# Optimization experiments

Measured on AMD Instinct MI355X. Metric: run time of the kernel, lower is better.

## Reference

```python
import jax, jax.numpy as jnp
import numpy as np

EMBED_DIM = 1024
NUM_HEADS = 16
SEQ = 2048
BATCH = 2


def setup_inputs() -> dict:
    key = jax.random.key(0)
    ks = jax.random.split(key, 9)
    E = EMBED_DIM
    gain = 1.0 / np.sqrt(2.0)  # xavier_uniform with gain 1/sqrt(2) (qkv_same_dim)
    limit = gain * np.sqrt(6.0 / (E + E))
    q = jax.random.normal(ks[0], (SEQ, BATCH, E), dtype=jnp.float32)
    k = jax.random.normal(ks[1], (SEQ, BATCH, E), dtype=jnp.float32)
    v = jax.random.normal(ks[2], (SEQ, BATCH, E), dtype=jnp.float32)
    Wq = jax.random.uniform(ks[3], (E, E), jnp.float32, -limit, limit)
    Wk = jax.random.uniform(ks[4], (E, E), jnp.float32, -limit, limit)
    Wv = jax.random.uniform(ks[5], (E, E), jnp.float32, -limit, limit)
    bq = jnp.zeros((E,), jnp.float32)
    bk = jnp.zeros((E,), jnp.float32)
    bv = jnp.zeros((E,), jnp.float32)
    return {"query": q, "key": k, "value": v,
            "Wq": Wq, "bq": bq, "Wk": Wk, "bk": bk, "Wv": Wv, "bv": bv}


def reference(query, key, value, Wq, bq, Wk, bk, Wv, bv):
    # Base Taylor attention path (norm_taylor=True, do_scale=True, has_out=False).
    L, B, E = query.shape
    H = NUM_HEADS
    hd = E // H
    scaling = E ** (-0.5)  # self.scaling = dim**-0.5, dim == embed_dim

    q = (query @ Wq + bq) * scaling          # (L, B, E)
    k = key @ Wk + bk                         # (S, B, E)
    v = value @ Wv + bv                       # (S, B, E)

    def split_heads(x):
        # (T, B, E) -> (B*H, T, hd)
        T = x.shape[0]
        return x.reshape(T, B * H, hd).transpose(1, 0, 2)

    qh, kh, vh = split_heads(q), split_heads(k), split_heads(v)

    # Taylor expansion of exp(qk) to first order: 1 + q.k
    attn = 1.0 + jnp.einsum('bld,bsd->bls', qh, kh)   # (B*H, L, S)
    attn = attn / attn.sum(axis=-1, keepdims=True)    # row-normalize
    out = jnp.einsum('bls,bsd->bld', attn, vh)        # (B*H, L, hd)
    out = out.transpose(1, 0, 2).reshape(L, B, E)     # (L, B, E)
    return out
```

## Files before the change

kernel.cpp:

```cpp
#include <hip/hip_runtime.h>
#include <hip/hip_bf16.h>

#define L_SEQ 2048
#define BATCH 2
#define ROWS 4096
#define E 1024
#define NH 16
#define HD 64

typedef __attribute__((ext_vector_type(4))) float f32x4;
typedef __attribute__((ext_vector_type(8))) __bf16 bf16x8;

#define SWZ(byt) ((byt) ^ ((((byt) >> 7) & 7) << 4))

__device__ __forceinline__ void gload16(const void* g, void* l) {
    __builtin_amdgcn_global_load_lds((const __attribute__((address_space(1))) void*)g,
                                     (__attribute__((address_space(3))) void*)l,
                                     16, 0, 0);
}

__global__ __launch_bounds__(256) void prep(const float* __restrict__ q,
                                            const float* __restrict__ k,
                                            const float* __restrict__ v,
                                            const float* __restrict__ Wq,
                                            const float* __restrict__ Wk,
                                            const float* __restrict__ Wv,
                                            __bf16* __restrict__ Xb,
                                            __bf16* __restrict__ Wt) {
    const int z = blockIdx.y;
    if (blockIdx.x < 2048) {
        const float* src = (z == 0) ? q : ((z == 1) ? k : v);
        __bf16* dst = Xb + (size_t)z * ROWS * E;
        const size_t i = ((size_t)blockIdx.x * 256 + threadIdx.x) * 8;
        const float4 a = *(const float4*)(src + i);
        const float4 b = *(const float4*)(src + i + 4);
        bf16x8 o;
        o[0] = (__bf16)a.x; o[1] = (__bf16)a.y; o[2] = (__bf16)a.z; o[3] = (__bf16)a.w;
        o[4] = (__bf16)b.x; o[5] = (__bf16)b.y; o[6] = (__bf16)b.z; o[7] = (__bf16)b.w;
        *(bf16x8*)(dst + i) = o;
        return;
    }
    const float* W = (z == 0) ? Wq : ((z == 1) ? Wk : Wv);
    __bf16* dst = Wt + (size_t)z * E * E;
    __shared__ __align__(16) float t[64][65];
    const int tt = blockIdx.x - 2048;
    const int n0 = (tt & 15) * 64, k0 = (tt >> 4) * 64;
    const int r = threadIdx.x >> 2, c4 = threadIdx.x & 3;
#pragma unroll
    for (int j = 0; j < 4; ++j) {
        const float4 vv = *(const float4*)&W[(size_t)(k0 + r) * E + n0 + c4 * 16 + j * 4];
        t[r][c4 * 16 + j * 4 + 0] = vv.x;
        t[r][c4 * 16 + j * 4 + 1] = vv.y;
        t[r][c4 * 16 + j * 4 + 2] = vv.z;
        t[r][c4 * 16 + j * 4 + 3] = vv.w;
    }
    __syncthreads();
    bf16x8 o0, o1;
#pragma unroll
    for (int j = 0; j < 8; ++j) {
        o0[j] = (__bf16)t[c4 * 16 + j][r];
        o1[j] = (__bf16)t[c4 * 16 + 8 + j][r];
    }
    *(bf16x8*)&dst[(size_t)(n0 + r) * E + k0 + c4 * 16] = o0;
    *(bf16x8*)&dst[(size_t)(n0 + r) * E + k0 + c4 * 16 + 8] = o1;
}

__device__ __forceinline__ void stage_tile(const __bf16* __restrict__ gsrc, int row0, int kcol,
                                           char* ldsdst, int wv, int ln) {
#pragma unroll
    for (int r = 0; r < 4; ++r) {
        const int rowg = row0 + r * 32 + wv * 8 + (ln >> 3);
        const int c16 = (ln & 7) ^ (ln >> 3);
        gload16(gsrc + (size_t)rowg * E + kcol + c16 * 8,
                ldsdst + r * 4096 + wv * 1024);
    }
}

__device__ __forceinline__ bf16x8 fragld(const char* base, int row, int kk, int kg) {
    return *(const bf16x8*)(base + row * 128 + ((((kk << 2) | kg) ^ (row & 7)) << 4));
}

#define PH_SYNC_BEGIN  __builtin_amdgcn_s_barrier(); \
                       asm volatile("s_waitcnt lgkmcnt(0)" ::: "memory"); \
                       __builtin_amdgcn_s_setprio(1);
#define PH_SYNC_END    __builtin_amdgcn_s_setprio(0); \
                       __builtin_amdgcn_s_barrier();

__global__ __launch_bounds__(256, 2) void gemm_qkv(const __bf16* __restrict__ Xb,
                                                   const __bf16* __restrict__ Wt,
                                                   const float* __restrict__ bq,
                                                   const float* __restrict__ bk,
                                                   const float* __restrict__ bv,
                                                   __bf16* __restrict__ Cb) {
    __shared__ __align__(16) char smem[65536];
    const int z = blockIdx.z;
    const __bf16* A = Xb + (size_t)z * ROWS * E;
    const __bf16* B = Wt + (size_t)z * E * E;
    __bf16* C = Cb + (size_t)z * ROWS * E;
    const float* bias = (z == 0) ? bq : ((z == 1) ? bk : bv);
    const float alpha = (z == 0) ? 0.03125f : 1.0f;
    const int m0 = blockIdx.x * 128, n0 = blockIdx.y * 128;
    const int tid = threadIdx.x, ln = tid & 63, wv = tid >> 6;
    const int lr = ln & 15, kg = ln >> 4;
    const int wm = (wv & 1) * 64, wn = (wv >> 1) * 64;
    char* LA0 = smem;            char* LA1 = smem + 16384;
    char* LB0 = smem + 32768;    char* LB1 = smem + 49152;

    stage_tile(A, m0, 0,  LA0, wv, ln);
    stage_tile(B, n0, 0,  LB0, wv, ln);
    stage_tile(A, m0, 64, LA1, wv, ln);
    asm volatile("s_waitcnt vmcnt(4)" ::: "memory");
    __builtin_amdgcn_s_barrier();

    f32x4 acc[4][4] = {};
    bf16x8 Af[4][2], Bf[2][2];

#define LOAD_B(nb) \
    _Pragma("unroll") for (int nn = 0; nn < 2; ++nn) \
    _Pragma("unroll") for (int kk = 0; kk < 2; ++kk) \
        Bf[nn][kk] = fragld(cB, wn + ((nb) + nn) * 16 + lr, kk, kg);
#define QUAD(q) \
    _Pragma("unroll") for (int m = 0; m < 4; ++m) \
    _Pragma("unroll") for (int nn = 0; nn < 2; ++nn) \
    _Pragma("unroll") for (int kk = 0; kk < 2; ++kk) \
        acc[m][2 * (q) + nn] = __builtin_amdgcn_mfma_f32_16x16x32_bf16(Af[m][kk], Bf[nn][kk], acc[m][2 * (q) + nn], 0, 0, 0);

    for (int T = 0; T < 16; ++T) {
        const char* cA = (T & 1) ? LA1 : LA0;
        const char* cB = (T & 1) ? LB1 : LB0;
        char* nB = (T & 1) ? LB0 : LB1;
        char* nA = (T & 1) ? LA1 : LA0;
#pragma unroll
        for (int m = 0; m < 4; ++m)
#pragma unroll
            for (int kk = 0; kk < 2; ++kk)
                Af[m][kk] = fragld(cA, wm + m * 16 + lr, kk, kg);
        LOAD_B(0);
        if (T < 15) stage_tile(B, n0, (T + 1) * 64, nB, wv, ln);
        PH_SYNC_BEGIN; QUAD(0); PH_SYNC_END;
        LOAD_B(2);
        if (T < 14) stage_tile(A, m0, (T + 2) * 64, nA, wv, ln);
        PH_SYNC_BEGIN; QUAD(1);
        __builtin_amdgcn_s_setprio(0);
        if (T < 14)       { asm volatile("s_waitcnt vmcnt(4)" ::: "memory"); }
        else if (T == 14) { asm volatile("s_waitcnt vmcnt(0)" ::: "memory"); }
        __builtin_amdgcn_s_barrier();
    }
#undef LOAD_B
#undef QUAD

#pragma unroll
    for (int m = 0; m < 4; ++m) {
        const int rbase = m0 + wm + m * 16 + kg * 4;
#pragma unroll
        for (int n = 0; n < 4; ++n) {
            const int col = n0 + wn + n * 16 + lr;
            const float bcol = bias[col];
#pragma unroll
            for (int rr = 0; rr < 4; ++rr)
                C[(size_t)(rbase + rr) * E + col] = (__bf16)((acc[m][n][rr] + bcol) * alpha);
        }
    }
}

__global__ __launch_bounds__(256) void reduce_kv(const __bf16* __restrict__ Kb,
                                                 const __bf16* __restrict__ Vb,
                                                 float* __restrict__ Mpart,
                                                 float* __restrict__ ksumP,
                                                 float* __restrict__ vsumP) {
    const int bh = blockIdx.x, b = bh >> 4, h = bh & 15;
    const int ts = blockIdx.y;
    const int t0 = ts * 128;
    __shared__ __align__(16) __bf16 sK[128 * 64];
    __shared__ __align__(16) __bf16 sV[128 * 64];
    __shared__ float red_k[4][64];
    __shared__ float red_v[4][64];
    const int tid = threadIdx.x;
    const int lane = tid & 63, wave = tid >> 6;
    const int lr = lane & 15, kg = lane >> 4;

    float vk[8] = {}, vv[8] = {};
    const int d0 = (tid & 7) * 8;
#pragma unroll
    for (int i = 0; i < 4; ++i) {
        const int t = i * 32 + (tid >> 3);
        const size_t g = (size_t)((t0 + t) * 2 + b) * E + h * 64 + d0;
        const bf16x8 kv = *(const bf16x8*)&Kb[g];
        const bf16x8 vvv = *(const bf16x8*)&Vb[g];
        const int lo = (t * 128 + d0 * 2) ^ (wave << 5);
        *(bf16x8*)((char*)sK + lo) = kv;
        *(bf16x8*)((char*)sV + lo) = vvv;
#pragma unroll
        for (int j = 0; j < 8; ++j) { vk[j] += (float)kv[j]; vv[j] += (float)vvv[j]; }
    }
#pragma unroll
    for (int m = 8; m <= 32; m <<= 1)
#pragma unroll
        for (int j = 0; j < 8; ++j) {
            vk[j] += __shfl_xor(vk[j], m, 64);
            vv[j] += __shfl_xor(vv[j], m, 64);
        }
    if (lane < 8)
#pragma unroll
        for (int j = 0; j < 8; ++j) {
            red_k[wave][lane * 8 + j] = vk[j];
            red_v[wave][lane * 8 + j] = vv[j];
        }
    __syncthreads();

    f32x4 acc[4] = {};
#pragma unroll
    for (int kt = 0; kt < 4; ++kt) {
        const int tb = kt * 32;
        bf16x8 afr, bfr[4];
        const char* pv = (const char*)sV + (((tb + kg * 8) * 128 + (wave * 16 + lr) * 2) ^ (kg << 5));
#pragma unroll
        for (int j = 0; j < 8; ++j) afr[j] = *(const __bf16*)(pv + j * 128);
#pragma unroll
        for (int ni = 0; ni < 4; ++ni) {
            const char* pk = (const char*)sK + (((tb + kg * 8) * 128 + (ni * 16 + lr) * 2) ^ (kg << 5));
#pragma unroll
            for (int j = 0; j < 8; ++j) bfr[ni][j] = *(const __bf16*)(pk + j * 128);
        }
#pragma unroll
        for (int ni = 0; ni < 4; ++ni)
            acc[ni] = __builtin_amdgcn_mfma_f32_16x16x32_bf16(afr, bfr[ni], acc[ni], 0, 0, 0);
    }

    float* Mp = Mpart + ((size_t)bh * 16 + ts) * 4096;
#pragma unroll
    for (int ni = 0; ni < 4; ++ni)
#pragma unroll
        for (int rr = 0; rr < 4; ++rr)
            Mp[(wave * 16 + kg * 4 + rr) * 64 + ni * 16 + lr] = acc[ni][rr];
    if (tid < 64)
        ksumP[(bh * 16 + ts) * 64 + tid] = red_k[0][tid] + red_k[1][tid] + red_k[2][tid] + red_k[3][tid];
    else if (tid < 128) {
        const int d = tid - 64;
        vsumP[(bh * 16 + ts) * 64 + d] = red_v[0][d] + red_v[1][d] + red_v[2][d] + red_v[3][d];
    }
}

__global__ __launch_bounds__(256) void combine_m(const float* __restrict__ Mpart,
                                                 const float* __restrict__ ksumP,
                                                 const float* __restrict__ vsumP,
                                                 float* __restrict__ Mt,
                                                 float* __restrict__ ksum,
                                                 float* __restrict__ vsum) {
    const int blk = blockIdx.x, tid = threadIdx.x;
    if (blk < 256) {
        const int e2 = (blk * 256 + tid) * 2;
        const int bh = e2 >> 12, r = e2 & 4095;
        const float* src = Mpart + (size_t)bh * 16 * 4096 + r;
        float s0 = 0.f, s1 = 0.f;
#pragma unroll
        for (int ts = 0; ts < 16; ++ts) {
            s0 += src[ts * 4096];
            s1 += src[ts * 4096 + 1];
        }
        Mt[(size_t)bh * 4096 + r] = s0;
        Mt[(size_t)bh * 4096 + r + 1] = s1;
    } else if (blk < 264) {
        const int idx = (blk - 256) * 256 + tid;
        const int bh = idx >> 6, d = idx & 63;
        float s = 0.f;
#pragma unroll
        for (int ts = 0; ts < 16; ++ts) s += ksumP[bh * 1024 + ts * 64 + d];
        ksum[idx] = s;
    } else {
        const int idx = (blk - 264) * 256 + tid;
        const int bh = idx >> 6, d = idx & 63;
        float s = 0.f;
#pragma unroll
        for (int ts = 0; ts < 16; ++ts) s += vsumP[bh * 1024 + ts * 64 + d];
        vsum[idx] = s;
    }
}

__global__ __launch_bounds__(256) void taylor_out(const __bf16* __restrict__ Qb,
                                                  const float* __restrict__ Mt,
                                                  const float* __restrict__ ksum,
                                                  const float* __restrict__ vsum,
                                                  float* __restrict__ out) {
    const int b = blockIdx.y;
    const int lblk = blockIdx.x * 16;
    const int tid = threadIdx.x, lane = tid & 63, wave = tid >> 6;
    const int lr = lane & 15, kg = lane >> 4;
    __shared__ __align__(16) __bf16 sM[4][4096];
    for (int hh = 0; hh < 4; ++hh) {
        __syncthreads();
#pragma unroll
        for (int i = 0; i < 8; ++i) {
            const int idx = i * 256 + tid;
            const int hseg = idx >> 9, rem = idx & 511;
            const float* src = &Mt[(size_t)(b * 16 + hseg * 4 + hh) * 4096 + rem * 8];
            const float4 mA = *(const float4*)src;
            const float4 mB = *(const float4*)(src + 4);
            bf16x8 o;
            o[0] = (__bf16)mA.x; o[1] = (__bf16)mA.y; o[2] = (__bf16)mA.z; o[3] = (__bf16)mA.w;
            o[4] = (__bf16)mB.x; o[5] = (__bf16)mB.y; o[6] = (__bf16)mB.z; o[7] = (__bf16)mB.w;
            *(bf16x8*)((char*)&sM[hseg][0] + SWZ(rem * 16)) = o;
        }
        __syncthreads();
        const int h = wave * 4 + hh;
        const int bh = b * 16 + h;
        const int rA = (lblk + lr) * 2 + b;
        const bf16x8 a0 = *(const bf16x8*)&Qb[(size_t)rA * E + h * 64 + kg * 8];
        const bf16x8 a1 = *(const bf16x8*)&Qb[(size_t)rA * E + h * 64 + 32 + kg * 8];
        float p = 0.f;
        const float* ks = &ksum[bh * 64];
#pragma unroll
        for (int j = 0; j < 8; ++j)
            p += (float)a0[j] * ks[kg * 8 + j] + (float)a1[j] * ks[32 + kg * 8 + j];
        p += __shfl_xor(p, 16, 64);
        p += __shfl_xor(p, 32, 64);
        const float Z = 2048.0f + p;
        f32x4 acc[4] = {};
#pragma unroll
        for (int ni = 0; ni < 4; ++ni) {
            const int byt0 = (ni * 16 + lr) * 128 + kg * 16;
            const bf16x8 b0 = *(const bf16x8*)((const char*)&sM[wave][0] + SWZ(byt0));
            const bf16x8 b1 = *(const bf16x8*)((const char*)&sM[wave][0] + SWZ(byt0 + 64));
            acc[ni] = __builtin_amdgcn_mfma_f32_16x16x32_bf16(a0, b0, acc[ni], 0, 0, 0);
            acc[ni] = __builtin_amdgcn_mfma_f32_16x16x32_bf16(a1, b1, acc[ni], 0, 0, 0);
        }
        float invZ[4];
#pragma unroll
        for (int rr = 0; rr < 4; ++rr) invZ[rr] = 1.0f / __shfl(Z, kg * 4 + rr, 64);
        const float* vs = &vsum[bh * 64];
#pragma unroll
        for (int ni = 0; ni < 4; ++ni)
#pragma unroll
            for (int rr = 0; rr < 4; ++rr) {
                const int l_out = lblk + kg * 4 + rr;
                out[(size_t)(l_out * 2 + b) * E + h * 64 + ni * 16 + lr] =
                    (vs[ni * 16 + lr] + acc[ni][rr]) * invZ[rr];
            }
    }
}

extern "C" void kernel_launch(void* const* d_in, const int* in_sizes, int n_in,
                              void* d_out, int out_size, void* d_ws, size_t ws_size,
                              hipStream_t stream) {
    const float* q  = (const float*)d_in[0];
    const float* k  = (const float*)d_in[1];
    const float* v  = (const float*)d_in[2];
    const float* Wq = (const float*)d_in[3];
    const float* bq = (const float*)d_in[4];
    const float* Wk = (const float*)d_in[5];
    const float* bk = (const float*)d_in[6];
    const float* Wv = (const float*)d_in[7];
    const float* bv = (const float*)d_in[8];
    float* out = (float*)d_out;
    char* w = (char*)d_ws;
    __bf16* Xb = (__bf16*)(w);
    __bf16* Wt = (__bf16*)(w + 25165824);
    __bf16* Cb = (__bf16*)(w + 31457280);
    float* Mt   = (float*)(w + 56623104);
    float* ksum = (float*)(w + 57147392);
    float* vsum = (float*)(w + 57155584);
    float* Mpart = (float*)(w);
    float* ksumP = (float*)(w + 8388608);
    float* vsumP = (float*)(w + 8519680);

    prep<<<dim3(2304, 3), 256, 0, stream>>>(q, k, v, Wq, Wk, Wv, Xb, Wt);
    gemm_qkv<<<dim3(32, 8, 3), 256, 0, stream>>>(Xb, Wt, bq, bk, bv, Cb);
    reduce_kv<<<dim3(32, 16), 256, 0, stream>>>(Cb + (size_t)ROWS * E,
                                                Cb + 2 * (size_t)ROWS * E, Mpart, ksumP, vsumP);
    combine_m<<<272, 256, 0, stream>>>(Mpart, ksumP, vsumP, Mt, ksum, vsum);
    taylor_out<<<dim3(128, 2), 256, 0, stream>>>(Cb, Mt, ksum, vsum, out);
}
```

Before: 71.71 us.

## Enlarge QKV GEMM tile to 256x128 with triple-buffered A in dynamic LDS

The QKV projection GEMM now gives each block a 256x128 output tile instead of 128x128, so each wave computes 128x64 with 32 accumulators. A is triple-buffered and B double-buffered in 128KB of dynamic shared memory, and fragment loads are restructured per k-slice. This halves the grid to 384 blocks and raises arithmetic intensity per LDS load, at the cost of one block per CU, higher register pressure, and fewer blocks to spread across the CUs.

Result: slower. 91.75 us (+27.9%).

```diff
diff --git a/kernel.cpp b/kernel.cpp
--- a/kernel.cpp
+++ b/kernel.cpp
@@ -65,8 +65,8 @@
     *(bf16x8*)&dst[(size_t)(n0 + r) * E + k0 + c4 * 16 + 8] = o1;
 }
 
-__device__ __forceinline__ void stage_tile(const __bf16* __restrict__ gsrc, int row0, int kcol,
-                                           char* ldsdst, int wv, int ln) {
+__device__ __forceinline__ void stageB(const __bf16* __restrict__ gsrc, int row0, int kcol,
+                                       char* ldsdst, int wv, int ln) {
 #pragma unroll
     for (int r = 0; r < 4; ++r) {
         const int rowg = row0 + r * 32 + wv * 8 + (ln >> 3);
@@ -76,6 +76,17 @@
     }
 }
 
+__device__ __forceinline__ void stageA(const __bf16* __restrict__ gsrc, int row0, int kcol,
+                                       char* ldsdst, int wv, int ln) {
+#pragma unroll
+    for (int r = 0; r < 8; ++r) {
+        const int rowg = row0 + r * 32 + wv * 8 + (ln >> 3);
+        const int c16 = (ln & 7) ^ (ln >> 3);
+        gload16(gsrc + (size_t)rowg * E + kcol + c16 * 8,
+                ldsdst + r * 4096 + wv * 1024);
+    }
+}
+
 __device__ __forceinline__ bf16x8 fragld(const char* base, int row, int kk, int kg) {
     return *(const bf16x8*)(base + row * 128 + ((((kk << 2) | kg) ^ (row & 7)) << 4));
 }
@@ -86,71 +97,66 @@
 #define PH_SYNC_END    __builtin_amdgcn_s_setprio(0); \
                        __builtin_amdgcn_s_barrier();
 
-__global__ __launch_bounds__(256, 2) void gemm_qkv(const __bf16* __restrict__ Xb,
+__global__ __launch_bounds__(256, 1) void gemm_qkv(const __bf16* __restrict__ Xb,
                                                    const __bf16* __restrict__ Wt,
                                                    const float* __restrict__ bq,
                                                    const float* __restrict__ bk,
                                                    const float* __restrict__ bv,
                                                    __bf16* __restrict__ Cb) {
-    __shared__ __align__(16) char smem[65536];
+    extern __shared__ __align__(16) char smem[];
     const int z = blockIdx.z;
     const __bf16* A = Xb + (size_t)z * ROWS * E;
     const __bf16* B = Wt + (size_t)z * E * E;
     __bf16* C = Cb + (size_t)z * ROWS * E;
     const float* bias = (z == 0) ? bq : ((z == 1) ? bk : bv);
     const float alpha = (z == 0) ? 0.03125f : 1.0f;
-    const int m0 = blockIdx.x * 128, n0 = blockIdx.y * 128;
+    const int m0 = blockIdx.x * 256, n0 = blockIdx.y * 128;
     const int tid = threadIdx.x, ln = tid & 63, wv = tid >> 6;
     const int lr = ln & 15, kg = ln >> 4;
-    const int wm = (wv & 1) * 64, wn = (wv >> 1) * 64;
-    char* LA0 = smem;            char* LA1 = smem + 16384;
-    char* LB0 = smem + 32768;    char* LB1 = smem + 49152;
-
-    stage_tile(A, m0, 0,  LA0, wv, ln);
-    stage_tile(B, n0, 0,  LB0, wv, ln);
-    stage_tile(A, m0, 64, LA1, wv, ln);
-    asm volatile("s_waitcnt vmcnt(4)" ::: "memory");
+    const int wm = (wv & 1) * 128, wn = (wv >> 1) * 64;
+    char* LB = smem + 98304;
+
+    stageA(A, m0, 0,  smem, wv, ln);
+    stageB(B, n0, 0,  LB, wv, ln);
+    stageA(A, m0, 64, smem + 32768, wv, ln);
+    asm volatile("s_waitcnt vmcnt(8)" ::: "memory");
     __builtin_amdgcn_s_barrier();
 
-    f32x4 acc[4][4] = {};
-    bf16x8 Af[4][2], Bf[2][2];
-
-#define LOAD_B(nb) \
-    _Pragma("unroll") for (int nn = 0; nn < 2; ++nn) \
-    _Pragma("unroll") for (int kk = 0; kk < 2; ++kk) \
-        Bf[nn][kk] = fragld(cB, wn + ((nb) + nn) * 16 + lr, kk, kg);
-#define QUAD(q) \
-    _Pragma("unroll") for (int m = 0; m < 4; ++m) \
-    _Pragma("unroll") for (int nn = 0; nn < 2; ++nn) \
-    _Pragma("unroll") for (int kk = 0; kk < 2; ++kk) \
-        acc[m][2 * (q) + nn] = __builtin_amdgcn_mfma_f32_16x16x32_bf16(Af[m][kk], Bf[nn][kk], acc[m][2 * (q) + nn], 0, 0, 0);
+    f32x4 acc[8][4] = {};
+
+#define FRAGS_AND_MFMA(kk)                                                        \
+    {                                                                             \
+        bf16x8 Af[8], Bf[4];                                                      \
+        _Pragma("unroll") for (int m = 0; m < 8; ++m)                             \
+            Af[m] = fragld(cA, wm + m * 16 + lr, kk, kg);                         \
+        _Pragma("unroll") for (int n = 0; n < 4; ++n)                             \
+            Bf[n] = fragld(cB, wn + n * 16 + lr, kk, kg);                         \
+        PH_SYNC_BEGIN;                                                            \
+        _Pragma("unroll") for (int m = 0; m < 8; ++m)                             \
+        _Pragma("unroll") for (int n = 0; n < 4; ++n)                             \
+            acc[m][n] = __builtin_amdgcn_mfma_f32_16x16x32_bf16(                  \
+                Af[m], Bf[n], acc[m][n], 0, 0, 0);                                \
+    }
 
     for (int T = 0; T < 16; ++T) {
-        const char* cA = (T & 1) ? LA1 : LA0;
-        const char* cB = (T & 1) ? LB1 : LB0;
-        char* nB = (T & 1) ? LB0 : LB1;
-        char* nA = (T & 1) ? LA1 : LA0;
-#pragma unroll
-        for (int m = 0; m < 4; ++m)
-#pragma unroll
-            for (int kk = 0; kk < 2; ++kk)
-                Af[m][kk] = fragld(cA, wm + m * 16 + lr, kk, kg);
-        LOAD_B(0);
-        if (T < 15) stage_tile(B, n0, (T + 1) * 64, nB, wv, ln);
-        PH_SYNC_BEGIN; QUAD(0); PH_SYNC_END;
-        LOAD_B(2);
-        if (T < 14) stage_tile(A, m0, (T + 2) * 64, nA, wv, ln);
-        PH_SYNC_BEGIN; QUAD(1);
+        const char* cA = smem + (T % 3) * 32768;
+        const char* cB = LB + (T & 1) * 16384;
+        char* nA = smem + ((T + 2) % 3) * 32768;
+        char* nB = LB + ((T + 1) & 1) * 16384;
+        if (T < 15) stageB(B, n0, (T + 1) * 64, nB, wv, ln);
+        FRAGS_AND_MFMA(0);
+        PH_SYNC_END;
+        if (T < 14) stageA(A, m0, (T + 2) * 64, nA, wv, ln);
+        FRAGS_AND_MFMA(1);
         __builtin_amdgcn_s_setprio(0);
-        if (T < 14)       { asm volatile("s_waitcnt vmcnt(4)" ::: "memory"); }
+        if (T < 14)       { asm volatile("s_waitcnt vmcnt(8)" ::: "memory"); }
         else if (T == 14) { asm volatile("s_waitcnt vmcnt(0)" ::: "memory"); }
         __builtin_amdgcn_s_barrier();
     }
-#undef LOAD_B
-#undef QUAD
-
-#pragma unroll
-    for (int m = 0; m < 4; ++m) {
+#undef FRAGS_AND_MFMA
+
+#pragma unroll
+    for (int m = 0; m < 8; ++m) {
         const int rbase = m0 + wm + m * 16 + kg * 4;
 #pragma unroll
         for (int n = 0; n < 4; ++n) {
@@ -363,8 +369,10 @@
     float* ksumP = (float*)(w + 8388608);
     float* vsumP = (float*)(w + 8519680);
 
+    hipFuncSetAttribute((const void*)gemm_qkv,
+                        hipFuncAttributeMaxDynamicSharedMemorySize, 131072);
     prep<<<dim3(2304, 3), 256, 0, stream>>>(q, k, v, Wq, Wk, Wv, Xb, Wt);
-    gemm_qkv<<<dim3(32, 8, 3), 256, 0, stream>>>(Xb, Wt, bq, bk, bv, Cb);
+    gemm_qkv<<<dim3(16, 8, 3), 256, 131072, stream>>>(Xb, Wt, bq, bk, bv, Cb);
     reduce_kv<<<dim3(32, 16), 256, 0, stream>>>(Cb + (size_t)ROWS * E,
                                                 Cb + 2 * (size_t)ROWS * E, Mpart, ksumP, vsumP);
     combine_m<<<272, 256, 0, stream>>>(Mpart, ksumP, vsumP, Mt, ksum, vsum);
```
